# Kernel tuning notes

Hardware: AMD Instinct MI355X
Metric: run time of the kernel (lower is better)

The kernel has to match this reference:

```python
import jax, jax.numpy as jnp
import numpy as np

NH = 8        # num_head
NP = 16       # num_att_points
MIN_A, MAX_A = 0.25, 0.75
EPS_REF = 1e-6
BN_EPS = 1e-5


def _conv1x1(x, w, b=None):
    # x: (B,C,H,W), w: (O,C)
    y = jnp.einsum('bchw,oc->bohw', x, w)
    if b is not None:
        y = y + b[None, :, None, None]
    return y


def _bilinear_sample(v, px, py, H, W):
    # v: (B,NH,hd,H*W); px,py pixel coords in [0,W-1]/[0,H-1], shape (B,NH,L,P)
    x0 = jnp.floor(px)
    y0 = jnp.floor(py)
    wx = (px - x0)[:, :, None, :, :]  # (B,NH,1,L,P)
    wy = (py - y0)[:, :, None, :, :]
    x0i = jnp.clip(x0.astype(jnp.int32), 0, W - 1)
    x1i = jnp.clip(x0.astype(jnp.int32) + 1, 0, W - 1)
    y0i = jnp.clip(y0.astype(jnp.int32), 0, H - 1)
    y1i = jnp.clip(y0.astype(jnp.int32) + 1, 0, H - 1)
    B, nh, hd, _ = v.shape
    L, P = px.shape[2], px.shape[3]

    def gather(yi, xi):
        idx = (yi * W + xi).reshape(B, nh, 1, L * P)
        return jnp.take_along_axis(v, idx, axis=3).reshape(B, nh, hd, L, P)

    top = (1.0 - wx) * gather(y0i, x0i) + wx * gather(y0i, x1i)
    bot = (1.0 - wx) * gather(y1i, x0i) + wx * gather(y1i, x1i)
    return (1.0 - wy) * top + wy * bot  # (B,NH,hd,L,P)


def _forward(feat_sd, w_size, b_size, w_anchor, b_anchor, w_value, b_value,
             w_att, b_att, w_out, bn_gamma, bn_beta, bn_mean, bn_var):
    B, C, H, W = feat_sd.shape
    L = H * W
    hd = C // NH

    memory = _conv1x1(feat_sd, w_value, b_value)  # (B,C,H,W)

    # reference window centers (same for every batch/head)
    yc = (jnp.arange(1, H + 1, dtype=feat_sd.dtype) - 0.5) / (H + EPS_REF)
    xc = (jnp.arange(1, W + 1, dtype=feat_sd.dtype) - 0.5) / (W + EPS_REF)
    cx = jnp.broadcast_to(xc[None, :], (H, W))
    cy = jnp.broadcast_to(yc[:, None], (H, W))
    center = jnp.stack([cx, cy], axis=-1).reshape(L, 2)  # (L,2) in (x,y)

    # per-head window sizes
    size = jnp.clip(jax.nn.sigmoid(_conv1x1(feat_sd, w_size, b_size)), MIN_A, MAX_A)
    size = size.reshape(B, NH, 2, L).transpose(0, 3, 1, 2)  # (B,L,NH,2)

    # per-point offsets in [0,1]
    off = jax.nn.sigmoid(_conv1x1(feat_sd, w_anchor, b_anchor))
    off = off.reshape(B, NH, NP, 2, L).transpose(0, 4, 1, 2, 3)  # (B,L,NH,NP,2)

    grid = center[None, :, None, None, :] - 0.5 * size[:, :, :, None, :] \
           + off * size[:, :, :, None, :]
    grid = jnp.clip(grid, 0.0, 1.0)  # (B,L,NH,NP,2), normalized (x,y)

    attn = _conv1x1(feat_sd, w_att, b_att).reshape(B, NH, NP, L).transpose(0, 3, 1, 2)
    attn = jax.nn.softmax(attn, axis=-1)  # (B,L,NH,NP)

    # sampling: align_corners=True bilinear -> pixel = g * (size-1)
    gx = grid[..., 0].transpose(0, 2, 1, 3) * (W - 1)  # (B,NH,L,NP)
    gy = grid[..., 1].transpose(0, 2, 1, 3) * (H - 1)
    v = memory.reshape(B, NH, hd, H * W)
    sampled = _bilinear_sample(v, gx, gy, H, W)  # (B,NH,hd,L,NP)

    out = jnp.einsum('bhdlp,blhp->blhd', sampled, attn)  # (B,L,NH,hd)
    out = out.reshape(B, L, C).transpose(0, 2, 1).reshape(B, C, H, W)

    out = _conv1x1(out, w_out, None)
    inv = jax.lax.rsqrt(bn_var + BN_EPS)
    out = (out - bn_mean[None, :, None, None]) * (bn_gamma * inv)[None, :, None, None] \
          + bn_beta[None, :, None, None]
    return out


def setup_inputs() -> dict:
    key = jax.random.key(0)
    B, C, H, W = 2, 256, 64, 96
    ks = jax.random.split(key, 8)
    n = lambda k, s: (jax.random.normal(k, s, jnp.float32) * 0.02)
    return {
        'feat_sd': jax.random.normal(ks[0], (B, C, H, W), jnp.float32),
        'w_size': n(ks[1], (NH * 2, C)), 'b_size': jnp.zeros((NH * 2,), jnp.float32),
        'w_anchor': n(ks[2], (NH * NP * 2, C)), 'b_anchor': jnp.zeros((NH * NP * 2,), jnp.float32),
        'w_value': n(ks[3], (C, C)), 'b_value': jnp.zeros((C,), jnp.float32),
        'w_att': n(ks[4], (NH * NP, C)), 'b_att': jnp.zeros((NH * NP,), jnp.float32),
        'w_out': n(ks[5], (C, C)),
        'bn_gamma': jnp.ones((C,), jnp.float32), 'bn_beta': jnp.zeros((C,), jnp.float32),
        'bn_mean': jnp.zeros((C,), jnp.float32), 'bn_var': jnp.ones((C,), jnp.float32),
    }


def reference(feat_sd, w_size, b_size, w_anchor, b_anchor, w_value, b_value,
              w_att, b_att, w_out, bn_gamma, bn_beta, bn_mean, bn_var):
    return _forward(feat_sd, w_size, b_size, w_anchor, b_anchor, w_value, b_value,
                    w_att, b_att, w_out, bn_gamma, bn_beta, bn_mean, bn_var)
```

## Files before the change

kernel.cpp:

```cpp
#include <hip/hip_runtime.h>
#include <math.h>

#define B_ 2
#define C_ 256
#define H_ 64
#define W_ 96
#define L_ (H_*W_)
#define NH_ 8
#define NP_ 16
#define HD_ 32
#define NTOT (B_*L_)
#define CO_ALL 656
#define CO_PAD 768
#define RAW_CH 400
#define LDK 72

typedef __attribute__((ext_vector_type(8))) short short8;
typedef __attribute__((ext_vector_type(4))) float f32x4;
typedef __attribute__((ext_vector_type(2))) float f32x2;

#define OFF_WALLBF 0
#define OFF_BALL   98304
#define OFF_WOUTBF 99072
#define OFF_FEATT  131840
#define OFF_MEMT   1704704
#define OFF_RAW    3277568
#define OFF_MIDT   8192768

__device__ __forceinline__ float sigmoidf_(float x) { return 1.f / (1.f + expf(-x)); }

__device__ __forceinline__ unsigned short f2bf(float x) {
    union { float f; unsigned int u; } v; v.f = x;
    unsigned int r = (v.u + 0x7fffu + ((v.u >> 16) & 1u)) >> 16;
    return (unsigned short)r;
}

__global__ __launch_bounds__(256) void prep(
        const float* __restrict__ wv, const float* __restrict__ bv,
        const float* __restrict__ wsz, const float* __restrict__ bsz,
        const float* __restrict__ wan, const float* __restrict__ ban,
        const float* __restrict__ wat, const float* __restrict__ bat,
        const float* __restrict__ wout, const float* __restrict__ feat,
        unsigned short* __restrict__ wallbf, float* __restrict__ ball,
        unsigned short* __restrict__ woutbf, unsigned short* __restrict__ featT) {
    __shared__ unsigned short tile[32][36];
    const int bid = blockIdx.x;
    const int t = threadIdx.x;
    if (bid < CO_PAD + C_) {
        const int o = bid, c = t;
        if (o < CO_PAD) {
            float v = 0.f, bvv = 0.f;
            if (o < 256)      { v = wv [(size_t)o*C_ + c];        bvv = bv [o]; }
            else if (o < 272) { v = wsz[(size_t)(o-256)*C_ + c];  bvv = bsz[o-256]; }
            else if (o < 528) { v = wan[(size_t)(o-272)*C_ + c];  bvv = ban[o-272]; }
            else if (o < 656) { v = wat[(size_t)(o-528)*C_ + c];  bvv = bat[o-528]; }
            wallbf[(size_t)o*C_ + c] = f2bf(v);
            if (c == 0) ball[o] = (o < CO_ALL) ? bvv : 0.f;
        } else {
            int r = o - CO_PAD;
            woutbf[(size_t)r*C_ + c] = f2bf(wout[(size_t)r*C_ + c]);
        }
        return;
    }
    const int tt = bid - (CO_PAD + C_);
    const int l0 = (tt % (L_/32)) * 32;
    const int c0 = ((tt / (L_/32)) & 7) * 32;
    const int b  = tt / ((L_/32) * 8);
    {
        const int c = t >> 3, l4 = (t & 7) * 4;
        float4 v = *(const float4*)(feat + ((size_t)b*C_ + c0 + c)*L_ + l0 + l4);
        tile[c][l4+0] = f2bf(v.x); tile[c][l4+1] = f2bf(v.y);
        tile[c][l4+2] = f2bf(v.z); tile[c][l4+3] = f2bf(v.w);
    }
    __syncthreads();
    {
        const int l = t >> 3, c4 = (t & 7) * 4;
        ushort4 v;
        v.x = tile[c4+0][l]; v.y = tile[c4+1][l];
        v.z = tile[c4+2][l]; v.w = tile[c4+3][l];
        *(ushort4*)(featT + ((size_t)(b*L_ + l0 + l))*C_ + c0 + c4) = v;
    }
}

__global__ __launch_bounds__(128) void gemm_a_mfma(const unsigned short* __restrict__ featT,
        const unsigned short* __restrict__ wallbf, const float* __restrict__ ball,
        unsigned short* __restrict__ memT, float* __restrict__ raw) {
    __shared__ short As[64 * LDK];
    __shared__ short Bs[64 * LDK];
    const int gid = blockIdx.x;
    const int xcd = gid & 7, jj = gid >> 3;
    const int yt = xcd * 24 + jj / 12;
    const int xt = jj % 12;
    const int m0 = xt * 64;
    const int n0 = yt * 64;
    const int b  = n0 / L_, l0 = n0 % L_;
    const int tid = threadIdx.x;
    const int wave = tid >> 6, lane = tid & 63;
    const int fr = lane & 15, fg = lane >> 4;
    f32x4 acc[2][4] = {};

    const unsigned short* fT = featT + ((size_t)(b*L_ + l0)) * C_;
    const int sr = tid >> 1;
    const int sko = (tid & 1) * 32;

    for (int k0 = 0; k0 < C_; k0 += 64) {
        const short8* ga = (const short8*)(wallbf + (size_t)(m0 + sr)*C_ + k0 + sko);
        const short8* gb = (const short8*)(fT + (size_t)sr*C_ + k0 + sko);
        short* la = As + sr*LDK + sko;
        short* lb = Bs + sr*LDK + sko;
        #pragma unroll
        for (int q = 0; q < 4; ++q) {
            *(short8*)(la + q*8) = ga[q];
            *(short8*)(lb + q*8) = gb[q];
        }
        __syncthreads();
        #pragma unroll
        for (int kk = 0; kk < 64; kk += 32) {
            short8 af[2], bfm[4];
            #pragma unroll
            for (int m = 0; m < 2; ++m)
                af[m] = *(const short8*)(As + (wave*32 + m*16 + fr)*LDK + kk + fg*8);
            #pragma unroll
            for (int n = 0; n < 4; ++n)
                bfm[n] = *(const short8*)(Bs + (n*16 + fr)*LDK + kk + fg*8);
            #pragma unroll
            for (int m = 0; m < 2; ++m)
                #pragma unroll
                for (int n = 0; n < 4; ++n)
                    acc[m][n] = __builtin_amdgcn_mfma_f32_16x16x32_bf16(af[m], bfm[n], acc[m][n], 0, 0, 0);
        }
        __syncthreads();
    }

    if (m0 < 256) {
        #pragma unroll
        for (int m = 0; m < 2; ++m) {
            const int ob = m0 + wave*32 + m*16 + fg*4;
            const int h = ob >> 5, d0 = ob & 31;
            const float b0 = ball[ob], b1 = ball[ob+1], b2 = ball[ob+2], b3 = ball[ob+3];
            #pragma unroll
            for (int n = 0; n < 4; ++n) {
                const int l = l0 + n*16 + fr;
                ushort4 v;
                v.x = f2bf(acc[m][n][0] + b0);
                v.y = f2bf(acc[m][n][1] + b1);
                v.z = f2bf(acc[m][n][2] + b2);
                v.w = f2bf(acc[m][n][3] + b3);
                *(ushort4*)(memT + ((size_t)(b*NH_ + h)*L_ + l)*HD_ + d0) = v;
            }
        }
    } else {
        #pragma unroll
        for (int m = 0; m < 2; ++m) {
            const int ob = m0 + wave*32 + m*16 + fg*4;
            #pragma unroll
            for (int n = 0; n < 4; ++n) {
                const int l = l0 + n*16 + fr;
                #pragma unroll
                for (int q = 0; q < 4; ++q) {
                    const int r = ob + q - 256;
                    if (r < RAW_CH)
                        raw[((size_t)(b*RAW_CH + r))*L_ + l] = acc[m][n][q] + ball[ob+q];
                }
            }
        }
    }
}

__global__ __launch_bounds__(256) void sample_kernel(
        const unsigned short* __restrict__ memT,
        const float* __restrict__ raw,
        unsigned short* __restrict__ midT) {
    __shared__ int4   tblo[16][16];
    __shared__ float4 tblw[16][16];
    __shared__ float  tile[16][33];
    const int blk = blockIdx.x;
    const int xcd = blk & 7;
    const int j   = blk >> 3;
    const int half = (j >= 384) ? 1 : 0;
    const int bh  = xcd * 2 + half;
    const int lt  = j - half * 384;
    const int h = bh & 7;
    const int b = bh >> 3;
    const int l0 = lt * 16;
    const int tid = threadIdx.x;

    {
        const int p    = tid & 15;
        const int lsub = tid >> 4;
        const int l = l0 + lsub;
        const float* rb = raw + (size_t)b * RAW_CH * L_ + l;
        float sx = fminf(fmaxf(sigmoidf_(rb[(h*2+0)*L_]), 0.25f), 0.75f);
        float sy = fminf(fmaxf(sigmoidf_(rb[(h*2+1)*L_]), 0.25f), 0.75f);
        float cx = ((l % W_) + 0.5f) / ((float)W_ + 1e-6f);
        float cy = ((l / W_) + 0.5f) / ((float)H_ + 1e-6f);
        float ox = sigmoidf_(rb[(16 + h*32 + p*2 + 0)*L_]);
        float oy = sigmoidf_(rb[(16 + h*32 + p*2 + 1)*L_]);
        float gx = fminf(fmaxf(cx - 0.5f*sx + ox*sx, 0.f), 1.f) * (float)(W_-1);
        float gy = fminf(fmaxf(cy - 0.5f*sy + oy*sy, 0.f), 1.f) * (float)(H_-1);
        float a = rb[(272 + h*16 + p)*L_];
        float m = a;
        #pragma unroll
        for (int dd = 8; dd >= 1; dd >>= 1) m = fmaxf(m, __shfl_xor(m, dd, 16));
        float e = expf(a - m);
        float s = e;
        #pragma unroll
        for (int dd = 8; dd >= 1; dd >>= 1) s += __shfl_xor(s, dd, 16);
        float aw = e / s;
        float x0f = floorf(gx), y0f = floorf(gy);
        int x0 = (int)x0f, y0 = (int)y0f;
        const float wx = gx - x0f, wy = gy - y0f;
        const int o00 = (y0*W_ + x0) * (HD_*2);
        const int dxb = (x0 < W_-1) ? (HD_*2) : 0;
        const int dyb = (y0 < H_-1) ? (W_*HD_*2) : 0;
        const float aiy = aw * (1.f - wy), awy = aw * wy;
        tblo[lsub][p] = make_int4(o00, o00 + dxb, o00 + dyb, o00 + dxb + dyb);
        tblw[lsub][p] = make_float4(aiy * (1.f - wx), aiy * wx,
                                    awy * (1.f - wx), awy * wx);
    }
    __syncthreads();

    const int wave = tid >> 6, lane = tid & 63;
    const int d2 = lane & 15;
    const int pg = lane >> 4;
    const int d2b = d2 * 4;
    const char* vbytes = (const char*)(memT + (size_t)(b*NH_ + h) * L_ * HD_);

    #pragma unroll
    for (int li = 0; li < 4; ++li) {
        const int lsub = wave*4 + li;
        uint u[16];
        float wcl[16];
        #pragma unroll
        for (int pi = 0; pi < 4; ++pi) {
            const int4   ob = tblo[lsub][pg*4 + pi];
            const float4 wv = tblw[lsub][pg*4 + pi];
            u[pi*4+0] = *(const uint*)(vbytes + (uint)(ob.x + d2b));
            u[pi*4+1] = *(const uint*)(vbytes + (uint)(ob.y + d2b));
            u[pi*4+2] = *(const uint*)(vbytes + (uint)(ob.z + d2b));
            u[pi*4+3] = *(const uint*)(vbytes + (uint)(ob.w + d2b));
            wcl[pi*4+0] = wv.x; wcl[pi*4+1] = wv.y;
            wcl[pi*4+2] = wv.z; wcl[pi*4+3] = wv.w;
        }
        f32x2 acc = {0.f, 0.f};
        #pragma unroll
        for (int k = 0; k < 16; ++k) {
            f32x2 v = { __uint_as_float(u[k] << 16), __uint_as_float(u[k] & 0xffff0000u) };
            acc += v * wcl[k];
        }
        acc.x += __shfl_xor(acc.x, 16);
        acc.y += __shfl_xor(acc.y, 16);
        acc.x += __shfl_xor(acc.x, 32);
        acc.y += __shfl_xor(acc.y, 32);
        if (pg == 0) { tile[lsub][d2*2] = acc.x; tile[lsub][d2*2+1] = acc.y; }
    }
    __syncthreads();
    if (tid < 128) {
        const int l = tid >> 3;
        const int c4 = (tid & 7) * 4;
        ushort4 v;
        v.x = f2bf(tile[l][c4+0]); v.y = f2bf(tile[l][c4+1]);
        v.z = f2bf(tile[l][c4+2]); v.w = f2bf(tile[l][c4+3]);
        *(ushort4*)(midT + ((size_t)(b*L_ + l0 + l))*C_ + h*HD_ + c4) = v;
    }
}

__global__ __launch_bounds__(128) void gemm_b_mfma(const unsigned short* __restrict__ midT,
        const unsigned short* __restrict__ woutbf,
        const float* __restrict__ gamma, const float* __restrict__ beta,
        const float* __restrict__ mean, const float* __restrict__ var,
        float* __restrict__ out) {
    __shared__ short As[64 * LDK];
    __shared__ short Bs[64 * LDK];
    const int gid = blockIdx.x;
    const int xcd = gid & 7, jj = gid >> 3;
    const int yt = xcd * 24 + jj / 4;
    const int xt = jj & 3;
    const int m0 = xt * 64;
    const int n0 = yt * 64;
    const int b  = n0 / L_, l0 = n0 % L_;
    const int tid = threadIdx.x;
    const int wave = tid >> 6, lane = tid & 63;
    const int fr = lane & 15, fg = lane >> 4;
    f32x4 acc[2][4] = {};

    const unsigned short* mT = midT + ((size_t)(b*L_ + l0)) * C_;
    const int sr = tid >> 1;
    const int sko = (tid & 1) * 32;

    for (int k0 = 0; k0 < C_; k0 += 64) {
        const short8* ga = (const short8*)(woutbf + (size_t)(m0 + sr)*C_ + k0 + sko);
        const short8* gb = (const short8*)(mT + (size_t)sr*C_ + k0 + sko);
        short* la = As + sr*LDK + sko;
        short* lb = Bs + sr*LDK + sko;
        #pragma unroll
        for (int q = 0; q < 4; ++q) {
            *(short8*)(la + q*8) = ga[q];
            *(short8*)(lb + q*8) = gb[q];
        }
        __syncthreads();
        #pragma unroll
        for (int kk = 0; kk < 64; kk += 32) {
            short8 af[2], bfm[4];
            #pragma unroll
            for (int m = 0; m < 2; ++m)
                af[m] = *(const short8*)(As + (wave*32 + m*16 + fr)*LDK + kk + fg*8);
            #pragma unroll
            for (int n = 0; n < 4; ++n)
                bfm[n] = *(const short8*)(Bs + (n*16 + fr)*LDK + kk + fg*8);
            #pragma unroll
            for (int m = 0; m < 2; ++m)
                #pragma unroll
                for (int n = 0; n < 4; ++n)
                    acc[m][n] = __builtin_amdgcn_mfma_f32_16x16x32_bf16(af[m], bfm[n], acc[m][n], 0, 0, 0);
        }
        __syncthreads();
    }

    #pragma unroll
    for (int m = 0; m < 2; ++m) {
        const int ob = m0 + wave*32 + m*16 + fg*4;
        float sc[4], mn[4], bt[4];
        #pragma unroll
        for (int q = 0; q < 4; ++q) {
            const int o = ob + q;
            sc[q] = gamma[o] * rsqrtf(var[o] + 1e-5f);
            mn[q] = mean[o]; bt[q] = beta[o];
        }
        #pragma unroll
        for (int n = 0; n < 4; ++n) {
            const int l = l0 + n*16 + fr;
            #pragma unroll
            for (int q = 0; q < 4; ++q)
                out[(size_t)b*C_*L_ + (size_t)(ob+q)*L_ + l] = (acc[m][n][q] - mn[q])*sc[q] + bt[q];
        }
    }
}

extern "C" void kernel_launch(void* const* d_in, const int* in_sizes, int n_in,
                              void* d_out, int out_size, void* d_ws, size_t ws_size,
                              hipStream_t stream) {
    const float* feat     = (const float*)d_in[0];
    const float* w_size   = (const float*)d_in[1];
    const float* b_size   = (const float*)d_in[2];
    const float* w_anchor = (const float*)d_in[3];
    const float* b_anchor = (const float*)d_in[4];
    const float* w_value  = (const float*)d_in[5];
    const float* b_value  = (const float*)d_in[6];
    const float* w_att    = (const float*)d_in[7];
    const float* b_att    = (const float*)d_in[8];
    const float* w_out    = (const float*)d_in[9];
    const float* bn_gamma = (const float*)d_in[10];
    const float* bn_beta  = (const float*)d_in[11];
    const float* bn_mean  = (const float*)d_in[12];
    const float* bn_var   = (const float*)d_in[13];

    float* ws = (float*)d_ws;
    unsigned short* wallbf = (unsigned short*)(ws + OFF_WALLBF);
    float*          ball   = ws + OFF_BALL;
    unsigned short* woutbf = (unsigned short*)(ws + OFF_WOUTBF);
    unsigned short* featT  = (unsigned short*)(ws + OFF_FEATT);
    unsigned short* memT   = (unsigned short*)(ws + OFF_MEMT);
    float*          raw    = ws + OFF_RAW;
    unsigned short* midT   = (unsigned short*)(ws + OFF_MIDT);

    prep<<<dim3(CO_PAD + C_ + (L_/32)*8*B_), dim3(256), 0, stream>>>(
        w_value, b_value, w_size, b_size, w_anchor, b_anchor, w_att, b_att,
        w_out, feat, wallbf, ball, woutbf, featT);
    gemm_a_mfma<<<dim3(8*288), dim3(128), 0, stream>>>(featT, wallbf, ball, memT, raw);
    sample_kernel<<<dim3(B_*NH_*(L_/16)), dim3(256), 0, stream>>>(memT, raw, midT);
    gemm_b_mfma<<<dim3(8*96), dim3(128), 0, stream>>>(
        midT, woutbf, bn_gamma, bn_beta, bn_mean, bn_var, (float*)d_out);
}
```

Baseline: 62.64 us.

## Restructure bilinear sampling lanes for 8-byte gathers and direct bf16 stores

The sampling kernel now packs offsets and weights into one int4 table split by x-corner. Each lane loads four bf16 channels (uint2) from two corners instead of two channels from four corners, so there are fewer, wider gather loads. The reduction runs across lanes via shuffles, and lanes 0-7 write bf16 results straight to global memory. This drops the shared-memory tile and the second barrier. In exchange the shuffle reduction takes three stages of four values, and the li loop is no longer forcibly unrolled, which can limit how many loads are in flight at once.

```diff
diff --git a/kernel.cpp b/kernel.cpp
--- a/kernel.cpp
+++ b/kernel.cpp
@@ -17,7 +17,6 @@
 
 typedef __attribute__((ext_vector_type(8))) short short8;
 typedef __attribute__((ext_vector_type(4))) float f32x4;
-typedef __attribute__((ext_vector_type(2))) float f32x2;
 
 #define OFF_WALLBF 0
 #define OFF_BALL   98304
@@ -171,9 +170,7 @@
         const unsigned short* __restrict__ memT,
         const float* __restrict__ raw,
         unsigned short* __restrict__ midT) {
-    __shared__ int4   tblo[16][16];
-    __shared__ float4 tblw[16][16];
-    __shared__ float  tile[16][33];
+    __shared__ int4 tbl[2][16][16];
     const int blk = blockIdx.x;
     const int xcd = blk & 7;
     const int j   = blk >> 3;
@@ -210,58 +207,58 @@
         float x0f = floorf(gx), y0f = floorf(gy);
         int x0 = (int)x0f, y0 = (int)y0f;
         const float wx = gx - x0f, wy = gy - y0f;
+        const float aiy = aw * (1.f - wy), awy = aw * wy;
         const int o00 = (y0*W_ + x0) * (HD_*2);
         const int dxb = (x0 < W_-1) ? (HD_*2) : 0;
-        const int dyb = (y0 < H_-1) ? (W_*HD_*2) : 0;
-        const float aiy = aw * (1.f - wy), awy = aw * wy;
-        tblo[lsub][p] = make_int4(o00, o00 + dxb, o00 + dyb, o00 + dxb + dyb);
-        tblw[lsub][p] = make_float4(aiy * (1.f - wx), aiy * wx,
-                                    awy * (1.f - wx), awy * wx);
+        const int o10 = o00 + ((y0 < H_-1) ? (W_*HD_*2) : 0);
+        tbl[0][lsub][p] = make_int4(o00, o10,
+                                    __float_as_int(aiy * (1.f - wx)),
+                                    __float_as_int(awy * (1.f - wx)));
+        tbl[1][lsub][p] = make_int4(o00 + dxb, o10 + dxb,
+                                    __float_as_int(aiy * wx),
+                                    __float_as_int(awy * wx));
     }
     __syncthreads();
 
     const int wave = tid >> 6, lane = tid & 63;
-    const int d2 = lane & 15;
+    const int d4 = lane & 7;
+    const int xh = (lane >> 3) & 1;
     const int pg = lane >> 4;
-    const int d2b = d2 * 4;
+    const int d4b = d4 * 8;
     const char* vbytes = (const char*)(memT + (size_t)(b*NH_ + h) * L_ * HD_);
 
-    #pragma unroll
     for (int li = 0; li < 4; ++li) {
         const int lsub = wave*4 + li;
-        uint u[16];
-        float wcl[16];
+        f32x4 acc = {0.f, 0.f, 0.f, 0.f};
         #pragma unroll
         for (int pi = 0; pi < 4; ++pi) {
-            const int4   ob = tblo[lsub][pg*4 + pi];
-            const float4 wv = tblw[lsub][pg*4 + pi];
-            u[pi*4+0] = *(const uint*)(vbytes + (uint)(ob.x + d2b));
-            u[pi*4+1] = *(const uint*)(vbytes + (uint)(ob.y + d2b));
-            u[pi*4+2] = *(const uint*)(vbytes + (uint)(ob.z + d2b));
-            u[pi*4+3] = *(const uint*)(vbytes + (uint)(ob.w + d2b));
-            wcl[pi*4+0] = wv.x; wcl[pi*4+1] = wv.y;
-            wcl[pi*4+2] = wv.z; wcl[pi*4+3] = wv.w;
-        }
-        f32x2 acc = {0.f, 0.f};
-        #pragma unroll
-        for (int k = 0; k < 16; ++k) {
-            f32x2 v = { __uint_as_float(u[k] << 16), __uint_as_float(u[k] & 0xffff0000u) };
-            acc += v * wcl[k];
-        }
-        acc.x += __shfl_xor(acc.x, 16);
-        acc.y += __shfl_xor(acc.y, 16);
-        acc.x += __shfl_xor(acc.x, 32);
-        acc.y += __shfl_xor(acc.y, 32);
-        if (pg == 0) { tile[lsub][d2*2] = acc.x; tile[lsub][d2*2+1] = acc.y; }
-    }
-    __syncthreads();
-    if (tid < 128) {
-        const int l = tid >> 3;
-        const int c4 = (tid & 7) * 4;
-        ushort4 v;
-        v.x = f2bf(tile[l][c4+0]); v.y = f2bf(tile[l][c4+1]);
-        v.z = f2bf(tile[l][c4+2]); v.w = f2bf(tile[l][c4+3]);
-        *(ushort4*)(midT + ((size_t)(b*L_ + l0 + l))*C_ + h*HD_ + c4) = v;
+            const int4 r = tbl[xh][lsub][pg*4 + pi];
+            const uint2 u0 = *(const uint2*)(vbytes + (uint)(r.x + d4b));
+            const uint2 u1 = *(const uint2*)(vbytes + (uint)(r.y + d4b));
+            const float w0 = __int_as_float(r.z);
+            const float w1 = __int_as_float(r.w);
+            acc.x += w0 * __uint_as_float(u0.x << 16);
+            acc.y += w0 * __uint_as_float(u0.x & 0xffff0000u);
+            acc.z += w0 * __uint_as_float(u0.y << 16);
+            acc.w += w0 * __uint_as_float(u0.y & 0xffff0000u);
+            acc.x += w1 * __uint_as_float(u1.x << 16);
+            acc.y += w1 * __uint_as_float(u1.x & 0xffff0000u);
+            acc.z += w1 * __uint_as_float(u1.y << 16);
+            acc.w += w1 * __uint_as_float(u1.y & 0xffff0000u);
+        }
+        #pragma unroll
+        for (int s = 8; s <= 32; s <<= 1) {
+            acc.x += __shfl_xor(acc.x, s);
+            acc.y += __shfl_xor(acc.y, s);
+            acc.z += __shfl_xor(acc.z, s);
+            acc.w += __shfl_xor(acc.w, s);
+        }
+        if (lane < 8) {
+            ushort4 v;
+            v.x = f2bf(acc.x); v.y = f2bf(acc.y);
+            v.z = f2bf(acc.z); v.w = f2bf(acc.w);
+            *(ushort4*)(midT + ((size_t)(b*L_ + l0 + lsub))*C_ + h*HD_ + lane*4) = v;
+        }
     }
 }
 
```

After: 71.38 us. 1.14x slower.
